# Kernel tuning notes

Hardware: AMD Instinct MI355X
Metric: run time of the kernel (lower is better)

## Reference

```python
import jax, jax.numpy as jnp
import numpy as np

N = 100000
E = 1600000
IN_C, HID_C, OUT_C = 512, 256, 64
K = 10
ALPHA = 0.1


def setup_inputs() -> dict:
    key = jax.random.key(0)
    k1, k2, k3, k4 = jax.random.split(key, 4)
    x = jax.random.normal(k1, (N, IN_C), dtype=jnp.float32)
    edge_index = jax.random.randint(k2, (2, E), 0, N, dtype=jnp.int64)
    # Glorot-ish scaled linear weights
    W1 = jax.random.normal(k3, (HID_C, IN_C), dtype=jnp.float32) / np.sqrt(IN_C)
    b1 = jnp.zeros((HID_C,), dtype=jnp.float32)
    W2 = jax.random.normal(k4, (OUT_C, HID_C), dtype=jnp.float32) / np.sqrt(HID_C)
    b2 = jnp.zeros((OUT_C,), dtype=jnp.float32)
    # PPR init: temp[k] = alpha*(1-alpha)^k, temp[K] = (1-alpha)^K
    temp = ALPHA * (1.0 - ALPHA) ** np.arange(K + 1)
    temp[-1] = (1.0 - ALPHA) ** K
    temp = jnp.asarray(temp, dtype=jnp.float32)
    return {"x": x, "edge_index": edge_index, "W1": W1, "b1": b1,
            "W2": W2, "b2": b2, "temp": temp}


def _gcn_norm(edge_index, num_nodes):
    # add self loops with weight 1, symmetric normalization D^-1/2 A D^-1/2
    loop = jnp.arange(num_nodes, dtype=edge_index.dtype)
    src = jnp.concatenate([edge_index[0], loop])
    dst = jnp.concatenate([edge_index[1], loop])
    w = jnp.ones(src.shape[0], dtype=jnp.float32)
    deg = jax.ops.segment_sum(w, dst, num_segments=num_nodes)
    dinv = jnp.where(deg > 0, jax.lax.rsqrt(deg), 0.0)
    norm = dinv[src] * w * dinv[dst]
    return src, dst, norm


def reference(x, edge_index, W1, b1, W2, b2, temp):
    # MLP (inference mode: dropout is identity)
    h = jax.nn.relu(x @ W1.T + b1)
    h = h @ W2.T + b2  # [N, OUT_C]

    src, dst, norm = _gcn_norm(edge_index, N)
    norm = norm[:, None]

    def step(carry, gamma):
        xk, hidden = carry
        xk = jax.ops.segment_sum(norm * xk[src], dst, num_segments=N)
        hidden = hidden + gamma * xk
        return (xk, hidden), None

    hidden0 = temp[0] * h
    (_, hidden), _ = jax.lax.scan(step, (h, hidden0), temp[1:])
    return hidden
```

## Files before the change

kernel.cpp:

```cpp
#include <hip/hip_runtime.h>

#define IN_C   512
#define HID_C  256
#define OUT_C  64
#define KSTEPS 10

typedef __attribute__((ext_vector_type(8))) short bf16x8;
typedef __attribute__((ext_vector_type(4))) float f32x4;

__device__ __forceinline__ uint f2bf(float f) {
    uint u = __float_as_uint(f);
    return (u + 0x7fffu + ((u >> 16) & 1u)) >> 16;
}
__device__ __forceinline__ float bfl(uint u) { return __uint_as_float(u << 16); }
__device__ __forceinline__ float bfh(uint u) { return __uint_as_float(u & 0xffff0000u); }

__global__ void k_init(int* __restrict__ cnt, int* __restrict__ fill, int n) {
    int i = blockIdx.x * blockDim.x + threadIdx.x;
    if (i < n) { cnt[i] = 0; fill[i] = 0; }
}

__global__ void k_hist(const int* __restrict__ ei, int* __restrict__ cnt, int E) {
    int e = blockIdx.x * blockDim.x + threadIdx.x;
    if (e < E) atomicAdd(&cnt[ei[E + e]], 1);
}

__global__ void k_dinv(const int* __restrict__ cnt, float* __restrict__ dinv, int n) {
    int i = blockIdx.x * blockDim.x + threadIdx.x;
    if (i < n) dinv[i] = rsqrtf((float)cnt[i] + 1.0f);
}

__global__ void k_scan1(const int* __restrict__ cnt, int* __restrict__ rowptr,
                        int* __restrict__ bsum, int n) {
    __shared__ int sh[256];
    int i = blockIdx.x * 256 + threadIdx.x;
    int v = (i < n) ? cnt[i] : 0;
    sh[threadIdx.x] = v;
    __syncthreads();
    for (int off = 1; off < 256; off <<= 1) {
        int t = (threadIdx.x >= off) ? sh[threadIdx.x - off] : 0;
        __syncthreads();
        sh[threadIdx.x] += t;
        __syncthreads();
    }
    if (i < n) rowptr[i + 1] = sh[threadIdx.x];
    if (threadIdx.x == 255) bsum[blockIdx.x] = sh[255];
}

__global__ void k_scan2(int* __restrict__ bsum, int nb) {
    __shared__ int sh[512];
    int t = threadIdx.x;
    int v = (t < nb) ? bsum[t] : 0;
    sh[t] = v;
    __syncthreads();
    for (int off = 1; off < 512; off <<= 1) {
        int u = (t >= off) ? sh[t - off] : 0;
        __syncthreads();
        sh[t] += u;
        __syncthreads();
    }
    int ex = (t == 0) ? 0 : sh[t - 1];
    if (t < nb) bsum[t] = ex;
}

__global__ void k_scan3(int* __restrict__ rowptr, const int* __restrict__ bsum, int n) {
    int i = blockIdx.x * blockDim.x + threadIdx.x;
    if (i < n) rowptr[i + 1] += bsum[i >> 8];
    if (i == 0) rowptr[0] = 0;
}

__global__ void k_scatter(const int* __restrict__ ei, const float* __restrict__ dinv,
                          const int* __restrict__ rowptr, int* __restrict__ fill,
                          int2* __restrict__ edges, int E) {
    int e = blockIdx.x * blockDim.x + threadIdx.x;
    if (e < E) {
        int s = ei[e], d = ei[E + e];
        float nv = dinv[s] * dinv[d];
        int pos = rowptr[d] + atomicAdd(&fill[d], 1);
        edges[pos] = make_int2(s, __float_as_int(nv));
    }
}

__global__ void k_prepw1(const float* __restrict__ W1, ushort* __restrict__ w1img) {
    int i = blockIdx.x * blockDim.x + threadIdx.x;
    if (i < HID_C * IN_C) {
        int t  = i >> 14;
        int rm = i & 16383;
        int nn = rm >> 6;
        int bd = (rm >> 3) & 7;
        int j  = rm & 7;
        int bq = bd ^ (nn & 7);
        w1img[i] = (ushort)f2bf(W1[nn * IN_C + t * 64 + bq * 8 + j]);
    }
}

__global__ void k_cvtw2(const float* __restrict__ W2, ushort* __restrict__ w2kt) {
    int i = blockIdx.x * blockDim.x + threadIdx.x;
    if (i < OUT_C * HID_C) {
        int o = i >> 8;
        int c = i & 255;
        int kb = c >> 3, j = c & 7;
        w2kt[((size_t)(kb * 64 + o)) * 8 + j] = (ushort)f2bf(W2[i]);
    }
}

__global__ __launch_bounds__(256, 4) void k_mlp(
    const float* __restrict__ x, const ushort* __restrict__ w1img,
    const float* __restrict__ b1, const ushort* __restrict__ w2kt,
    const float* __restrict__ b2, const float* __restrict__ temp,
    ushort* __restrict__ h, float* __restrict__ out, int n)
{
    __shared__ uint4 smem4[2560];
    char* smem = (char*)smem4;

    const int tid = threadIdx.x;
    const int lane = tid & 63;
    const int w    = tid >> 6;
    const int l15  = lane & 15;
    const int l4   = lane >> 4;
    const int row0 = blockIdx.x * 64;

    f32x4 acc[4][4];
#pragma unroll
    for (int i = 0; i < 4; ++i)
#pragma unroll
        for (int j = 0; j < 4; ++j) acc[i][j] = (f32x4){0.f, 0.f, 0.f, 0.f};

    for (int k0 = 0; k0 < IN_C; k0 += 64) {
        const char* w1c = (const char*)w1img + (size_t)(k0 >> 6) * 32768;
#pragma unroll
        for (int it = 0; it < 8; ++it) {
            int base = it * 4096 + w * 1024;
            __builtin_amdgcn_global_load_lds(
                (const __attribute__((address_space(1))) void*)(w1c + base + lane * 16),
                (__attribute__((address_space(3))) void*)(smem + base),
                16, 0, 0);
        }
#pragma unroll
        for (int it = 0; it < 4; ++it) {
            int f  = tid + it * 256;
            int r  = f >> 4;
            int c4 = f & 15;
            int gr = row0 + r; if (gr >= n) gr = n - 1;
            float4 v = *(const float4*)(x + (size_t)gr * IN_C + k0 + c4 * 4);
            uint p0 = f2bf(v.x) | (f2bf(v.y) << 16);
            uint p1 = f2bf(v.z) | (f2bf(v.w) << 16);
            int boff = (c4 * 8) ^ ((r & 7) << 4);
            *(uint2*)(smem + 32768 + r * 128 + boff) = make_uint2(p0, p1);
        }
        __syncthreads();

#pragma unroll
        for (int kk = 0; kk < 2; ++kk) {
            bf16x8 af[4], bfr[4];
            int kb = kk * 4 + l4;
#pragma unroll
            for (int rf = 0; rf < 4; ++rf) {
                int r = rf * 16 + l15;
                af[rf] = *(const bf16x8*)(smem + 32768 + r * 128 + ((kb ^ (r & 7)) << 4));
            }
#pragma unroll
            for (int nf = 0; nf < 4; ++nf) {
                int nn = w * 64 + nf * 16 + l15;
                bfr[nf] = *(const bf16x8*)(smem + nn * 128 + ((kb ^ (nn & 7)) << 4));
            }
#pragma unroll
            for (int rf = 0; rf < 4; ++rf)
#pragma unroll
                for (int nf = 0; nf < 4; ++nf)
                    acc[rf][nf] = __builtin_amdgcn_mfma_f32_16x16x32_bf16(
                        af[rf], bfr[nf], acc[rf][nf], 0, 0, 0);
        }
        __syncthreads();
    }

    float bias1[4];
#pragma unroll
    for (int nf = 0; nf < 4; ++nf) bias1[nf] = b1[w * 64 + nf * 16 + l15];
#pragma unroll
    for (int rf = 0; rf < 4; ++rf)
#pragma unroll
        for (int nf = 0; nf < 4; ++nf)
#pragma unroll
            for (int j = 0; j < 4; ++j) {
                int r = rf * 16 + l4 * 4 + j;
                int c = w * 64 + nf * 16 + l15;
                float v = fmaxf(acc[rf][nf][j] + bias1[nf], 0.f);
                int byte = r * 512 + ((((c >> 3) ^ (r & 7))) << 4) + (c & 7) * 2;
                *(ushort*)(smem + byte) = (ushort)f2bf(v);
            }
    __syncthreads();

    f32x4 acc2[4];
#pragma unroll
    for (int nf = 0; nf < 4; ++nf) acc2[nf] = (f32x4){0.f, 0.f, 0.f, 0.f};
#pragma unroll
    for (int kk = 0; kk < 8; ++kk) {
        int r = w * 16 + l15;
        int kb = kk * 4 + l4;
        bf16x8 a = *(const bf16x8*)(smem + r * 512 + ((kb ^ (r & 7)) << 4));
#pragma unroll
        for (int nf = 0; nf < 4; ++nf) {
            bf16x8 bb = *(const bf16x8*)(w2kt + ((size_t)kb * 64 + nf * 16 + l15) * 8);
            acc2[nf] = __builtin_amdgcn_mfma_f32_16x16x32_bf16(a, bb, acc2[nf], 0, 0, 0);
        }
    }

    float t0 = temp[0];
#pragma unroll
    for (int nf = 0; nf < 4; ++nf) {
        int c = nf * 16 + l15;
        float bias = b2[c];
#pragma unroll
        for (int j = 0; j < 4; ++j) {
            int gr = row0 + w * 16 + l4 * 4 + j;
            if (gr < n) {
                float v = acc2[nf][j] + bias;
                h[(size_t)gr * OUT_C + c]   = (ushort)f2bf(v);
                out[(size_t)gr * OUT_C + c] = t0 * v;
            }
        }
    }
}

__global__ __launch_bounds__(256) void k_prop(
    const int* __restrict__ rowptr, const int2* __restrict__ edges,
    const ushort* __restrict__ cur, ushort* __restrict__ nxt,
    float* __restrict__ out, const float* __restrict__ dinv,
    const float* __restrict__ temp, int kcur, int do_rmw, int do_nxt, int n)
{
    const int lane = threadIdx.x & 63;
    const int g    = lane >> 3;
    const int sl   = lane & 7;
    const int wid  = (blockIdx.x * blockDim.x + threadIdx.x) >> 6;
    const int nw   = (gridDim.x * blockDim.x) >> 6;
    const float gc = temp[kcur];
    const float gp = temp[kcur - 1];

    for (int base = wid * 8; base < n; base += nw * 8) {
        int d = base + g;
        bool act = d < n;
        int dd = act ? d : (n - 1);
        int b = rowptr[dd];
        int en = act ? rowptr[dd + 1] : b;
        float di = dinv[dd];
        size_t rowoff = (size_t)dd * OUT_C + sl * 8;

        uint4 sraw = *(const uint4*)(cur + rowoff);
        float c0 = bfl(sraw.x), c1 = bfh(sraw.x), c2 = bfl(sraw.y), c3 = bfh(sraw.y),
              c4 = bfl(sraw.z), c5 = bfh(sraw.z), c6 = bfl(sraw.w), c7 = bfh(sraw.w);
        float s = di * di;
        float a0 = s * c0, a1 = s * c1, a2 = s * c2, a3 = s * c3,
              a4 = s * c4, a5 = s * c5, a6 = s * c6, a7 = s * c7;

        int i = b;
        for (; i + 4 <= en; i += 4) {
            int2 e0 = edges[i], e1 = edges[i + 1], e2 = edges[i + 2], e3 = edges[i + 3];
            uint4 r0 = *(const uint4*)(cur + (size_t)e0.x * OUT_C + sl * 8);
            uint4 r1 = *(const uint4*)(cur + (size_t)e1.x * OUT_C + sl * 8);
            uint4 r2 = *(const uint4*)(cur + (size_t)e2.x * OUT_C + sl * 8);
            uint4 r3 = *(const uint4*)(cur + (size_t)e3.x * OUT_C + sl * 8);
            float w0 = __int_as_float(e0.y), w1 = __int_as_float(e1.y);
            float w2 = __int_as_float(e2.y), w3 = __int_as_float(e3.y);
            a0 = fmaf(w0, bfl(r0.x), a0); a1 = fmaf(w0, bfh(r0.x), a1);
            a2 = fmaf(w0, bfl(r0.y), a2); a3 = fmaf(w0, bfh(r0.y), a3);
            a4 = fmaf(w0, bfl(r0.z), a4); a5 = fmaf(w0, bfh(r0.z), a5);
            a6 = fmaf(w0, bfl(r0.w), a6); a7 = fmaf(w0, bfh(r0.w), a7);
            a0 = fmaf(w1, bfl(r1.x), a0); a1 = fmaf(w1, bfh(r1.x), a1);
            a2 = fmaf(w1, bfl(r1.y), a2); a3 = fmaf(w1, bfh(r1.y), a3);
            a4 = fmaf(w1, bfl(r1.z), a4); a5 = fmaf(w1, bfh(r1.z), a5);
            a6 = fmaf(w1, bfl(r1.w), a6); a7 = fmaf(w1, bfh(r1.w), a7);
            a0 = fmaf(w2, bfl(r2.x), a0); a1 = fmaf(w2, bfh(r2.x), a1);
            a2 = fmaf(w2, bfl(r2.y), a2); a3 = fmaf(w2, bfh(r2.y), a3);
            a4 = fmaf(w2, bfl(r2.z), a4); a5 = fmaf(w2, bfh(r2.z), a5);
            a6 = fmaf(w2, bfl(r2.w), a6); a7 = fmaf(w2, bfh(r2.w), a7);
            a0 = fmaf(w3, bfl(r3.x), a0); a1 = fmaf(w3, bfh(r3.x), a1);
            a2 = fmaf(w3, bfl(r3.y), a2); a3 = fmaf(w3, bfh(r3.y), a3);
            a4 = fmaf(w3, bfl(r3.z), a4); a5 = fmaf(w3, bfh(r3.z), a5);
            a6 = fmaf(w3, bfl(r3.w), a6); a7 = fmaf(w3, bfh(r3.w), a7);
        }
        for (; i < en; ++i) {
            int2 e = edges[i];
            uint4 r0 = *(const uint4*)(cur + (size_t)e.x * OUT_C + sl * 8);
            float w0 = __int_as_float(e.y);
            a0 = fmaf(w0, bfl(r0.x), a0); a1 = fmaf(w0, bfh(r0.x), a1);
            a2 = fmaf(w0, bfl(r0.y), a2); a3 = fmaf(w0, bfh(r0.y), a3);
            a4 = fmaf(w0, bfl(r0.z), a4); a5 = fmaf(w0, bfh(r0.z), a5);
            a6 = fmaf(w0, bfl(r0.w), a6); a7 = fmaf(w0, bfh(r0.w), a7);
        }

        if (act) {
            if (do_nxt) {
                uint4 pk;
                pk.x = f2bf(a0) | (f2bf(a1) << 16);
                pk.y = f2bf(a2) | (f2bf(a3) << 16);
                pk.z = f2bf(a4) | (f2bf(a5) << 16);
                pk.w = f2bf(a6) | (f2bf(a7) << 16);
                *(uint4*)(nxt + rowoff) = pk;
            }
            if (do_rmw) {
                float4* op = (float4*)(out + rowoff);
                float4 v0 = op[0], v1 = op[1];
                v0.x += gp * c0 + gc * a0; v0.y += gp * c1 + gc * a1;
                v0.z += gp * c2 + gc * a2; v0.w += gp * c3 + gc * a3;
                v1.x += gp * c4 + gc * a4; v1.y += gp * c5 + gc * a5;
                v1.z += gp * c6 + gc * a6; v1.w += gp * c7 + gc * a7;
                op[0] = v0; op[1] = v1;
            }
        }
    }
}

extern "C" void kernel_launch(void* const* d_in, const int* in_sizes, int n_in,
                              void* d_out, int out_size, void* d_ws, size_t ws_size,
                              hipStream_t stream)
{
    const float* x    = (const float*)d_in[0];
    const int*   ei   = (const int*)d_in[1];
    const float* W1   = (const float*)d_in[2];
    const float* b1   = (const float*)d_in[3];
    const float* W2   = (const float*)d_in[4];
    const float* b2   = (const float*)d_in[5];
    const float* temp = (const float*)d_in[6];
    float* out = (float*)d_out;

    const int N = in_sizes[0] / IN_C;
    const int E = in_sizes[1] / 2;

    char* ws = (char*)d_ws;
    ushort* bufA  = (ushort*)ws;
    ushort* bufB  = bufA + (size_t)N * OUT_C;
    int2*   edges = (int2*)(bufB + (size_t)N * OUT_C);
    ushort* w1img = (ushort*)(edges + E);
    ushort* w2kt  = w1img + HID_C * IN_C;
    float*  dinv  = (float*)(w2kt + OUT_C * HID_C);
    int*    cnt    = (int*)(dinv + N);
    int*    fill   = cnt + N;
    int*    rowptr = fill + N;
    int*    bsum   = rowptr + (N + 16);

    const int nbN = (N + 255) / 256;
    const int nbE = (E + 255) / 256;

    k_init   <<<nbN, 256, 0, stream>>>(cnt, fill, N);
    k_hist   <<<nbE, 256, 0, stream>>>(ei, cnt, E);
    k_dinv   <<<nbN, 256, 0, stream>>>(cnt, dinv, N);
    k_scan1  <<<nbN, 256, 0, stream>>>(cnt, rowptr, bsum, N);
    k_scan2  <<<1,   512, 0, stream>>>(bsum, nbN);
    k_scan3  <<<nbN, 256, 0, stream>>>(rowptr, bsum, N);
    k_scatter<<<nbE, 256, 0, stream>>>(ei, dinv, rowptr, fill, edges, E);
    k_prepw1 <<<(HID_C * IN_C + 255) / 256, 256, 0, stream>>>(W1, w1img);
    k_cvtw2  <<<(OUT_C * HID_C + 255) / 256, 256, 0, stream>>>(W2, w2kt);

    k_mlp<<<(N + 63) / 64, 256, 0, stream>>>(x, w1img, b1, w2kt, b2, temp, bufA, out, N);

    ushort* cur = bufA;
    ushort* nxt = bufB;
    for (int k = 1; k <= KSTEPS; ++k) {
        int do_rmw = (k % 2 == 0) ? 1 : 0;
        int do_nxt = (k < KSTEPS) ? 1 : 0;
        k_prop<<<2048, 256, 0, stream>>>(rowptr, edges, cur, nxt, out, dinv,
                                         temp, k, do_rmw, do_nxt, N);
        ushort* t = cur; cur = nxt; nxt = t;
    }
}
```

Baseline: 585.3 us.

## Sort CSR edges by source within rows via two-pass counting sort

Builds the destination CSR in two passes: edges are first bucketed by source node, then scattered into destination rows. Because the second scatter reads edges in source order, each row's neighbor list tends to be ordered by source, which is meant to improve cache locality of the feature gathers in the propagation kernel. This adds an extra histogram, scan and scatter pass plus workspace for a second edge array, and atomic slot allocation means the ordering is only approximate.

Result: slower. 757.5 us (+29.4%).

```diff
diff --git a/kernel.cpp b/kernel.cpp
--- a/kernel.cpp
+++ b/kernel.cpp
@@ -15,14 +15,14 @@
 __device__ __forceinline__ float bfl(uint u) { return __uint_as_float(u << 16); }
 __device__ __forceinline__ float bfh(uint u) { return __uint_as_float(u & 0xffff0000u); }
 
-__global__ void k_init(int* __restrict__ cnt, int* __restrict__ fill, int n) {
-    int i = blockIdx.x * blockDim.x + threadIdx.x;
-    if (i < n) { cnt[i] = 0; fill[i] = 0; }
-}
-
-__global__ void k_hist(const int* __restrict__ ei, int* __restrict__ cnt, int E) {
+__global__ void k_init(int* __restrict__ a, int* __restrict__ b, int n) {
+    int i = blockIdx.x * blockDim.x + threadIdx.x;
+    if (i < n) { a[i] = 0; b[i] = 0; }
+}
+
+__global__ void k_hist_idx(const int* __restrict__ idx, int* __restrict__ cnt, int E) {
     int e = blockIdx.x * blockDim.x + threadIdx.x;
-    if (e < E) atomicAdd(&cnt[ei[E + e]], 1);
+    if (e < E) atomicAdd(&cnt[idx[e]], 1);
 }
 
 __global__ void k_dinv(const int* __restrict__ cnt, float* __restrict__ dinv, int n) {
@@ -30,7 +30,7 @@
     if (i < n) dinv[i] = rsqrtf((float)cnt[i] + 1.0f);
 }
 
-__global__ void k_scan1(const int* __restrict__ cnt, int* __restrict__ rowptr,
+__global__ void k_scan1(const int* __restrict__ cnt, int* __restrict__ ptr,
                         int* __restrict__ bsum, int n) {
     __shared__ int sh[256];
     int i = blockIdx.x * 256 + threadIdx.x;
@@ -43,7 +43,7 @@
         sh[threadIdx.x] += t;
         __syncthreads();
     }
-    if (i < n) rowptr[i + 1] = sh[threadIdx.x];
+    if (i < n) ptr[i + 1] = sh[threadIdx.x];
     if (threadIdx.x == 255) bsum[blockIdx.x] = sh[255];
 }
 
@@ -63,21 +63,31 @@
     if (t < nb) bsum[t] = ex;
 }
 
-__global__ void k_scan3(int* __restrict__ rowptr, const int* __restrict__ bsum, int n) {
-    int i = blockIdx.x * blockDim.x + threadIdx.x;
-    if (i < n) rowptr[i + 1] += bsum[i >> 8];
-    if (i == 0) rowptr[0] = 0;
-}
-
-__global__ void k_scatter(const int* __restrict__ ei, const float* __restrict__ dinv,
-                          const int* __restrict__ rowptr, int* __restrict__ fill,
-                          int2* __restrict__ edges, int E) {
+__global__ void k_scan3(int* __restrict__ ptr, const int* __restrict__ bsum, int n) {
+    int i = blockIdx.x * blockDim.x + threadIdx.x;
+    if (i < n) ptr[i + 1] += bsum[i >> 8];
+    if (i == 0) ptr[0] = 0;
+}
+
+__global__ void k_scatterA(const int* __restrict__ ei, const int* __restrict__ srcptr,
+                           int* __restrict__ fillA, int2* __restrict__ edgesA, int E) {
     int e = blockIdx.x * blockDim.x + threadIdx.x;
     if (e < E) {
         int s = ei[e], d = ei[E + e];
-        float nv = dinv[s] * dinv[d];
-        int pos = rowptr[d] + atomicAdd(&fill[d], 1);
-        edges[pos] = make_int2(s, __float_as_int(nv));
+        int pos = srcptr[s] + atomicAdd(&fillA[s], 1);
+        edgesA[pos] = make_int2(s, d);
+    }
+}
+
+__global__ void k_scatterB(const int2* __restrict__ edgesA, const float* __restrict__ dinv,
+                           const int* __restrict__ rowptr, int* __restrict__ fill,
+                           int2* __restrict__ edges, int E) {
+    int j = blockIdx.x * blockDim.x + threadIdx.x;
+    if (j < E) {
+        int2 sd = edgesA[j];
+        float nv = dinv[sd.x] * dinv[sd.y];
+        int pos = rowptr[sd.y] + atomicAdd(&fill[sd.y], 1);
+        edges[pos] = make_int2(sd.x, __float_as_int(nv));
     }
 }
 
@@ -328,29 +338,40 @@
     const int E = in_sizes[1] / 2;
 
     char* ws = (char*)d_ws;
-    ushort* bufA  = (ushort*)ws;
-    ushort* bufB  = bufA + (size_t)N * OUT_C;
-    int2*   edges = (int2*)(bufB + (size_t)N * OUT_C);
-    ushort* w1img = (ushort*)(edges + E);
-    ushort* w2kt  = w1img + HID_C * IN_C;
-    float*  dinv  = (float*)(w2kt + OUT_C * HID_C);
-    int*    cnt    = (int*)(dinv + N);
-    int*    fill   = cnt + N;
-    int*    rowptr = fill + N;
-    int*    bsum   = rowptr + (N + 16);
+    ushort* bufA   = (ushort*)ws;
+    ushort* bufB   = bufA + (size_t)N * OUT_C;
+    int2*   edges  = (int2*)(bufB + (size_t)N * OUT_C);
+    int2*   edgesA = edges + E;
+    ushort* w1img  = (ushort*)(edgesA + E);
+    ushort* w2kt   = w1img + HID_C * IN_C;
+    float*  dinv   = (float*)(w2kt + OUT_C * HID_C);
+    int*    cnt     = (int*)(dinv + N);
+    int*    fill    = cnt + N;
+    int*    rowptr  = fill + N;
+    int*    bsum    = rowptr + (N + 16);
+    int*    cntA    = bsum + 512;
+    int*    fillA   = cntA + N;
+    int*    srcptr  = fillA + N;
+    int*    bsumA   = srcptr + (N + 16);
 
     const int nbN = (N + 255) / 256;
     const int nbE = (E + 255) / 256;
 
-    k_init   <<<nbN, 256, 0, stream>>>(cnt, fill, N);
-    k_hist   <<<nbE, 256, 0, stream>>>(ei, cnt, E);
-    k_dinv   <<<nbN, 256, 0, stream>>>(cnt, dinv, N);
-    k_scan1  <<<nbN, 256, 0, stream>>>(cnt, rowptr, bsum, N);
-    k_scan2  <<<1,   512, 0, stream>>>(bsum, nbN);
-    k_scan3  <<<nbN, 256, 0, stream>>>(rowptr, bsum, N);
-    k_scatter<<<nbE, 256, 0, stream>>>(ei, dinv, rowptr, fill, edges, E);
-    k_prepw1 <<<(HID_C * IN_C + 255) / 256, 256, 0, stream>>>(W1, w1img);
-    k_cvtw2  <<<(OUT_C * HID_C + 255) / 256, 256, 0, stream>>>(W2, w2kt);
+    k_init    <<<nbN, 256, 0, stream>>>(cnt, fill, N);
+    k_init    <<<nbN, 256, 0, stream>>>(cntA, fillA, N);
+    k_hist_idx<<<nbE, 256, 0, stream>>>(ei + E, cnt, E);
+    k_hist_idx<<<nbE, 256, 0, stream>>>(ei, cntA, E);
+    k_dinv    <<<nbN, 256, 0, stream>>>(cnt, dinv, N);
+    k_scan1   <<<nbN, 256, 0, stream>>>(cnt, rowptr, bsum, N);
+    k_scan2   <<<1,   512, 0, stream>>>(bsum, nbN);
+    k_scan3   <<<nbN, 256, 0, stream>>>(rowptr, bsum, N);
+    k_scan1   <<<nbN, 256, 0, stream>>>(cntA, srcptr, bsumA, N);
+    k_scan2   <<<1,   512, 0, stream>>>(bsumA, nbN);
+    k_scan3   <<<nbN, 256, 0, stream>>>(srcptr, bsumA, N);
+    k_scatterA<<<nbE, 256, 0, stream>>>(ei, srcptr, fillA, edgesA, E);
+    k_scatterB<<<nbE, 256, 0, stream>>>(edgesA, dinv, rowptr, fill, edges, E);
+    k_prepw1  <<<(HID_C * IN_C + 255) / 256, 256, 0, stream>>>(W1, w1img);
+    k_cvtw2   <<<(OUT_C * HID_C + 255) / 256, 256, 0, stream>>>(W2, w2kt);
 
     k_mlp<<<(N + 63) / 64, 256, 0, stream>>>(x, w1img, b1, w2kt, b2, temp, bufA, out, N);
 
```
